# Performance work log

Hardware: AMD Instinct MI355X
Metric: run time of the kernel (lower is better)

The kernel has to match this reference:

```python
import jax, jax.numpy as jnp
import numpy as np

GRID_SIZE = 5
SPLINE_ORDER = 3
NUM_BASIS = GRID_SIZE + SPLINE_ORDER  # 8
GRID = jnp.linspace(-1.0, 1.0, GRID_SIZE + 2 * SPLINE_ORDER + 1)  # [12]
EPS = 1e-6


def bspline_basis(x):
    """Iterative Cox-de Boor. x: [...]; returns [..., NUM_BASIS]."""
    xe = x[..., None]
    # order-0 indicator basis: [..., G-1]
    B = ((xe >= GRID[:-1]) & (xe < GRID[1:])).astype(x.dtype)
    for k in range(1, SPLINE_ORDER + 1):
        nb = B.shape[-1] - 1
        g_i = GRID[:nb]
        g_i1 = GRID[1:1 + nb]
        g_ik = GRID[k:k + nb]
        g_ik1 = GRID[k + 1:k + 1 + nb]
        dl = g_ik - g_i
        dr = g_ik1 - g_i1
        left = jnp.where(dl > EPS, (xe - g_i) / jnp.where(dl > EPS, dl, 1.0), 0.0) * B[..., :nb]
        right = jnp.where(dr > EPS, (g_ik1 - xe) / jnp.where(dr > EPS, dr, 1.0), 0.0) * B[..., 1:nb + 1]
        B = left + right
    return B[..., :NUM_BASIS]


def setup_inputs() -> dict:
    key = jax.random.key(0)
    k1, k2 = jax.random.split(key)
    x = jax.random.normal(k1, (8192, 512), dtype=jnp.float32)
    spline_coeffs = jax.random.normal(k2, (512, 512, NUM_BASIS), dtype=jnp.float32) * 0.1
    return {"x": x, "spline_coeffs": spline_coeffs}


def reference(x, spline_coeffs):
    xn = jnp.tanh(x)                       # [B, in]
    basis = bspline_basis(xn)              # [B, in, K]
    # output[b, o] = sum_{i,k} coeffs[o, i, k] * basis[b, i, k]
    return jnp.einsum('bik,oik->bo', basis, spline_coeffs)
```

## Files before the change

kernel.cpp:

```cpp
#include <hip/hip_runtime.h>
#include <hip/hip_bf16.h>
#include <stdint.h>


#define M_TOTAL 8192
#define N_DIM   512
#define K_DIM   4096
#define BM 128
#define BN 128
#define BK 64
#define NT_HALF 32
#define GRP_LDS 65536
#define BUF_HALF 32768

typedef __attribute__((ext_vector_type(8))) short short8;
typedef __attribute__((ext_vector_type(4))) float f32x4;

typedef const __attribute__((address_space(1))) uint32_t ga_u32;
typedef __attribute__((address_space(3))) uint32_t ls_u32;

__device__ __forceinline__ void gload_lds16(const void* g, void* l) {
  __builtin_amdgcn_global_load_lds((ga_u32*)(uintptr_t)g,
                                   (ls_u32*)(uint32_t)(uintptr_t)l, 16, 0, 0);
}

__device__ __forceinline__ uint32_t f2bf(float f) {
  uint32_t u = __builtin_bit_cast(uint32_t, f);
  return (u + 0x7FFFu + ((u >> 16) & 1u)) >> 16;
}

__device__ __forceinline__ void basis_slots(float xv, uint32_t o[4]) {
  xv = fminf(15.f, fmaxf(-15.f, xv));
  float e  = __expf(2.0f * xv);
  float t  = (e - 1.0f) * __builtin_amdgcn_rcpf(e + 1.0f);
  float uf = (t + 1.0f) * 5.5f;
  int   c  = (int)uf;  c = c > 10 ? 10 : c;
  float u  = uf - (float)c;
  float u2 = u * u, u3 = u2 * u, om = 1.0f - u;
  float w0 = om * om * om * (1.0f / 6.0f);
  float w1 = (3.0f * u3 - 6.0f * u2 + 4.0f) * (1.0f / 6.0f);
  float w2 = (-3.0f * u3 + 3.0f * u2 + 3.0f * u + 1.0f) * (1.0f / 6.0f);
  float w3 = u3 * (1.0f / 6.0f);
  uint32_t p01 = f2bf(w0) | (f2bf(w1) << 16);
  uint32_t p23 = f2bf(w2) | (f2bf(w3) << 16);
  uint64_t W = (uint64_t)p01 | ((uint64_t)p23 << 32);
  int d = c - 3;
  uint64_t lo = (d < 0) ? (W >> ((-d) * 16))
              : ((d < 4) ? (W << (d * 16)) : 0ull);
  uint64_t hi = (d <= 0) ? 0ull
              : ((d < 4) ? (W >> ((4 - d) * 16)) : (W << ((d - 4) * 16)));
  o[0] = (uint32_t)lo; o[1] = (uint32_t)(lo >> 32);
  o[2] = (uint32_t)hi; o[3] = (uint32_t)(hi >> 32);
}

__global__ __launch_bounds__(256) void basis_kernel(const float* __restrict__ x,
                                                    __hip_bfloat16* __restrict__ A,
                                                    int total) {
  int idx = blockIdx.x * 256 + threadIdx.x;
  if (idx >= total) return;
  uint32_t o[4];
  basis_slots(x[idx], o);
  reinterpret_cast<int4*>(A)[idx] = make_int4(o[0], o[1], o[2], o[3]);
}

__global__ __launch_bounds__(256) void cvt_kernel(const float* __restrict__ c,
                                                  __hip_bfloat16* __restrict__ Bt,
                                                  int total8) {
  int idx = blockIdx.x * 256 + threadIdx.x;
  if (idx >= total8) return;
  const float4* cp = reinterpret_cast<const float4*>(c) + (size_t)idx * 2;
  float4 a = cp[0], b = cp[1];
  union { unsigned short us[8]; int4 v; } pk;
  pk.us[0] = (unsigned short)f2bf(a.x); pk.us[1] = (unsigned short)f2bf(a.y);
  pk.us[2] = (unsigned short)f2bf(a.z); pk.us[3] = (unsigned short)f2bf(a.w);
  pk.us[4] = (unsigned short)f2bf(b.x); pk.us[5] = (unsigned short)f2bf(b.y);
  pk.us[6] = (unsigned short)f2bf(b.z); pk.us[7] = (unsigned short)f2bf(b.w);
  reinterpret_cast<int4*>(Bt)[idx] = pk.v;
}

__global__ __launch_bounds__(512) void gemm_kernel(
    const __hip_bfloat16* __restrict__ A,
    const __hip_bfloat16* __restrict__ Bt,
    float* __restrict__ C) {
  __shared__ char lds[2 * GRP_LDS];

  const int tid   = threadIdx.x;
  const int wid   = tid >> 6;
  const int lane  = tid & 63;
  const int quad  = lane >> 4;
  const int l16   = lane & 15;
  const int kgrp  = wid >> 2;
  const int w2    = wid & 3;
  const int waveM = w2 >> 1, waveN = w2 & 1;
  const int tg    = tid & 255;

  const int b  = blockIdx.x;
  const int q  = b >> 3;
  const int mt = (b & 7) * 8 + (q >> 2);
  const int nt = q & 3;
  const int m0 = mt * BM;
  const int n0 = nt * BN;

  char* grp = lds + kgrp * GRP_LDS;

  uint32_t aGlob[4], bGlob[4], sOff[4];
#pragma unroll
  for (int t = 0; t < 4; ++t) {
    int s = t * 256 + tg, row = s >> 3, p = s & 7, cc = p ^ (row & 7);
    sOff[t]  = (uint32_t)s * 16u;
    aGlob[t] = (uint32_t)(m0 + row) * K_DIM + (uint32_t)cc * 8u
             + (uint32_t)kgrp * 2048u;
    bGlob[t] = (uint32_t)(n0 + row) * K_DIM + (uint32_t)cc * 8u
             + (uint32_t)kgrp * 2048u;
  }

  uint32_t aOff[2][4], bOff[2][4];
#pragma unroll
  for (int kk = 0; kk < 2; ++kk) {
    int c = kk * 4 + quad;
#pragma unroll
    for (int mi = 0; mi < 4; ++mi) {
      int row = waveM * 64 + mi * 16 + l16;
      aOff[kk][mi] = (uint32_t)(row * 8 + (c ^ (row & 7))) * 16u;
    }
#pragma unroll
    for (int ni = 0; ni < 4; ++ni) {
      int row = waveN * 64 + ni * 16 + l16;
      bOff[kk][ni] = 16384u + (uint32_t)(row * 8 + (c ^ (row & 7))) * 16u;
    }
  }

  f32x4 acc[4][4];
#pragma unroll
  for (int mi = 0; mi < 4; ++mi)
#pragma unroll
    for (int ni = 0; ni < 4; ++ni)
      acc[mi][ni] = (f32x4){0.f, 0.f, 0.f, 0.f};

#pragma unroll
  for (int t = 0; t < 4; ++t) {
    gload_lds16(A + aGlob[t], grp + sOff[t]);
    gload_lds16(Bt + bGlob[t], grp + 16384 + sOff[t]);
  }

  for (int it = 0; it < NT_HALF; ++it) {
    const int cur = it & 1;
    char* bufc = grp + cur * BUF_HALF;
    __syncthreads();
    if (it + 1 < NT_HALF) {
      char* bufn = grp + (1 - cur) * BUF_HALF;
      uint32_t kt = (uint32_t)(it + 1) * BK;
#pragma unroll
      for (int t = 0; t < 4; ++t) {
        gload_lds16(A + aGlob[t] + kt, bufn + sOff[t]);
        gload_lds16(Bt + bGlob[t] + kt, bufn + 16384 + sOff[t]);
      }
    }
#pragma unroll
    for (int kk = 0; kk < 2; ++kk) {
      short8 af[4], bf[4];
#pragma unroll
      for (int mi = 0; mi < 4; ++mi)
        af[mi] = *reinterpret_cast<const short8*>(bufc + aOff[kk][mi]);
#pragma unroll
      for (int ni = 0; ni < 4; ++ni)
        bf[ni] = *reinterpret_cast<const short8*>(bufc + bOff[kk][ni]);
#pragma unroll
      for (int mi = 0; mi < 4; ++mi)
#pragma unroll
        for (int ni = 0; ni < 4; ++ni)
          acc[mi][ni] = __builtin_amdgcn_mfma_f32_16x16x32_bf16(
              af[mi], bf[ni], acc[mi][ni], 0, 0, 0);
    }
  }

  __syncthreads();
  if (kgrp == 1) {
#pragma unroll
    for (int mi = 0; mi < 4; ++mi)
#pragma unroll
      for (int ni = 0; ni < 4; ++ni) {
        int f = mi * 4 + ni;
        *reinterpret_cast<f32x4*>(lds + w2 * 16384 + f * 1024 + lane * 16) =
            acc[mi][ni];
      }
  }
  __syncthreads();
  if (kgrp == 0) {
#pragma unroll
    for (int mi = 0; mi < 4; ++mi) {
#pragma unroll
      for (int ni = 0; ni < 4; ++ni) {
        int f = mi * 4 + ni;
        f32x4 other = *reinterpret_cast<f32x4*>(
            lds + w2 * 16384 + f * 1024 + lane * 16);
        f32x4 s = acc[mi][ni] + other;
        int col = n0 + waveN * 64 + ni * 16 + l16;
#pragma unroll
        for (int r = 0; r < 4; ++r) {
          int row = m0 + waveM * 64 + mi * 16 + quad * 4 + r;
          C[(size_t)row * N_DIM + col] = s[r];
        }
      }
    }
  }
}

extern "C" void kernel_launch(void* const* d_in, const int* in_sizes, int n_in,
                              void* d_out, int out_size, void* d_ws, size_t ws_size,
                              hipStream_t stream) {
  const float* x    = (const float*)d_in[0];
  const float* coef = (const float*)d_in[1];
  float* out = (float*)d_out;

  __hip_bfloat16* Bt = (__hip_bfloat16*)d_ws;
  __hip_bfloat16* A  = (__hip_bfloat16*)((char*)d_ws + (size_t)4 * 1024 * 1024);

  const int total8 = N_DIM * K_DIM / 8;
  cvt_kernel<<<(total8 + 255) / 256, 256, 0, stream>>>(coef, Bt, total8);

  const int total = M_TOTAL * 512;
  basis_kernel<<<total / 256, 256, 0, stream>>>(x, A, total);

  gemm_kernel<<<(M_TOTAL / BM) * (N_DIM / BN), 512, 0, stream>>>(A, Bt, out);
}
```

Baseline: 118.2 us.

## Use 256x256 tiles with 4-way split-K, interleaved prefetch, and a separate reduce

The GEMM moves from 128x128 tiles with an in-block two-group K split to 256x256 tiles with a 4-way split-K across blocks. Each block writes fp32 partial sums to workspace, and a new reduce kernel adds them. The main loop splits each K step into four MFMA phases, with global-to-LDS prefetch spread between phases and s_setprio around the MFMAs to overlap loads with compute. This aims for higher arithmetic intensity and better latency hiding. The cost is 64 MB of partial-sum traffic plus an extra kernel launch, and higher register pressure from 128 accumulators per thread.

```diff
diff --git a/kernel.cpp b/kernel.cpp
--- a/kernel.cpp
+++ b/kernel.cpp
@@ -6,12 +6,12 @@
 #define M_TOTAL 8192
 #define N_DIM   512
 #define K_DIM   4096
-#define BM 128
-#define BN 128
+#define BM 256
+#define BN 256
 #define BK 64
-#define NT_HALF 32
-#define GRP_LDS 65536
-#define BUF_HALF 32768
+#define NSPLIT 4
+#define NT 16
+#define BUF_SZ 65536
 
 typedef __attribute__((ext_vector_type(8))) short short8;
 typedef __attribute__((ext_vector_type(4))) float f32x4;
@@ -78,131 +78,191 @@
   reinterpret_cast<int4*>(Bt)[idx] = pk.v;
 }
 
-__global__ __launch_bounds__(512) void gemm_kernel(
+__global__ __launch_bounds__(512, 2) void gemm_kernel(
     const __hip_bfloat16* __restrict__ A,
     const __hip_bfloat16* __restrict__ Bt,
-    float* __restrict__ C) {
-  __shared__ char lds[2 * GRP_LDS];
+    float* __restrict__ P) {
+  __shared__ char lds[2 * BUF_SZ];
 
   const int tid   = threadIdx.x;
   const int wid   = tid >> 6;
   const int lane  = tid & 63;
   const int quad  = lane >> 4;
   const int l16   = lane & 15;
-  const int kgrp  = wid >> 2;
-  const int w2    = wid & 3;
-  const int waveM = w2 >> 1, waveN = w2 & 1;
-  const int tg    = tid & 255;
-
-  const int b  = blockIdx.x;
-  const int q  = b >> 3;
-  const int mt = (b & 7) * 8 + (q >> 2);
-  const int nt = q & 3;
+  const int waveM = wid >> 2;
+  const int waveN = wid & 3;
+
+  const int b     = blockIdx.x;
+  const int xcd   = b & 7;
+  const int r     = b >> 3;
+  const int mt    = xcd * 4 + (r >> 3);
+  const int q     = r & 7;
+  const int nt    = q & 1;
+  const int split = q >> 1;
   const int m0 = mt * BM;
   const int n0 = nt * BN;
-
-  char* grp = lds + kgrp * GRP_LDS;
-
-  uint32_t aGlob[4], bGlob[4], sOff[4];
+  const uint32_t kb = (uint32_t)split * 1024u;
+
+  uint32_t aSrc[4], aDst[4], bSrc[4], bDst[4];
 #pragma unroll
   for (int t = 0; t < 4; ++t) {
-    int s = t * 256 + tg, row = s >> 3, p = s & 7, cc = p ^ (row & 7);
-    sOff[t]  = (uint32_t)s * 16u;
-    aGlob[t] = (uint32_t)(m0 + row) * K_DIM + (uint32_t)cc * 8u
-             + (uint32_t)kgrp * 2048u;
-    bGlob[t] = (uint32_t)(n0 + row) * K_DIM + (uint32_t)cc * 8u
-             + (uint32_t)kgrp * 2048u;
-  }
-
-  uint32_t aOff[2][4], bOff[2][4];
+    int p    = tid & 7;
+    int arow = ((t & 1) << 7) + ((t >> 1) << 6) + (tid >> 3);
+    aSrc[t] = (uint32_t)(m0 + arow) * K_DIM + (uint32_t)((p ^ (arow & 7)) * 8)
+            + kb;
+    aDst[t] = (uint32_t)(arow * 8 + p) * 16u;
+    int brow = t * 64 + (tid >> 3);
+    bSrc[t] = (uint32_t)(n0 + brow) * K_DIM + (uint32_t)((p ^ (brow & 7)) * 8)
+            + kb;
+    bDst[t] = 32768u + (uint32_t)(brow * 8 + p) * 16u;
+  }
+
+  uint32_t aOff[2][2][4], bOff[2][4];
 #pragma unroll
   for (int kk = 0; kk < 2; ++kk) {
     int c = kk * 4 + quad;
 #pragma unroll
-    for (int mi = 0; mi < 4; ++mi) {
-      int row = waveM * 64 + mi * 16 + l16;
-      aOff[kk][mi] = (uint32_t)(row * 8 + (c ^ (row & 7))) * 16u;
-    }
+    for (int mh = 0; mh < 2; ++mh)
+#pragma unroll
+      for (int mi = 0; mi < 4; ++mi) {
+        int row = waveM * 128 + mh * 64 + mi * 16 + l16;
+        aOff[kk][mh][mi] = (uint32_t)(row * 8 + (c ^ (row & 7))) * 16u;
+      }
 #pragma unroll
     for (int ni = 0; ni < 4; ++ni) {
       int row = waveN * 64 + ni * 16 + l16;
-      bOff[kk][ni] = 16384u + (uint32_t)(row * 8 + (c ^ (row & 7))) * 16u;
-    }
-  }
-
-  f32x4 acc[4][4];
-#pragma unroll
-  for (int mi = 0; mi < 4; ++mi)
+      bOff[kk][ni] = 32768u + (uint32_t)(row * 8 + (c ^ (row & 7))) * 16u;
+    }
+  }
+
+  f32x4 acc[2][4][4];
+#pragma unroll
+  for (int mh = 0; mh < 2; ++mh)
+#pragma unroll
+    for (int mi = 0; mi < 4; ++mi)
+#pragma unroll
+      for (int ni = 0; ni < 4; ++ni)
+        acc[mh][mi][ni] = (f32x4){0.f, 0.f, 0.f, 0.f};
+
+#pragma unroll
+  for (int t = 0; t < 4; ++t) gload_lds16(Bt + bSrc[t], lds + bDst[t]);
+#pragma unroll
+  for (int t = 0; t < 4; ++t) gload_lds16(A + aSrc[t], lds + aDst[t]);
+  asm volatile("s_waitcnt vmcnt(2)" ::: "memory");
+  __builtin_amdgcn_s_barrier();
+
+  for (int it = 0; it < NT; ++it) {
+    char* bufc = lds + (it & 1) * BUF_SZ;
+    char* bufn = lds + ((it + 1) & 1) * BUF_SZ;
+    const uint32_t kt = (uint32_t)(it + 1) * BK;
+    const bool more = (it + 1) < NT;
+    short8 af[4], bfr[4];
+
+#pragma unroll
+    for (int mi = 0; mi < 4; ++mi)
+      af[mi] = *reinterpret_cast<const short8*>(bufc + aOff[0][0][mi]);
 #pragma unroll
     for (int ni = 0; ni < 4; ++ni)
-      acc[mi][ni] = (f32x4){0.f, 0.f, 0.f, 0.f};
-
-#pragma unroll
-  for (int t = 0; t < 4; ++t) {
-    gload_lds16(A + aGlob[t], grp + sOff[t]);
-    gload_lds16(Bt + bGlob[t], grp + 16384 + sOff[t]);
-  }
-
-  for (int it = 0; it < NT_HALF; ++it) {
-    const int cur = it & 1;
-    char* bufc = grp + cur * BUF_HALF;
-    __syncthreads();
-    if (it + 1 < NT_HALF) {
-      char* bufn = grp + (1 - cur) * BUF_HALF;
-      uint32_t kt = (uint32_t)(it + 1) * BK;
-#pragma unroll
-      for (int t = 0; t < 4; ++t) {
-        gload_lds16(A + aGlob[t] + kt, bufn + sOff[t]);
-        gload_lds16(Bt + bGlob[t] + kt, bufn + 16384 + sOff[t]);
+      bfr[ni] = *reinterpret_cast<const short8*>(bufc + bOff[0][ni]);
+    if (more) {
+      gload_lds16(Bt + bSrc[0] + kt, bufn + bDst[0]);
+      gload_lds16(Bt + bSrc[1] + kt, bufn + bDst[1]);
+      asm volatile("s_waitcnt vmcnt(2)" ::: "memory");
+    } else {
+      asm volatile("s_waitcnt vmcnt(0)" ::: "memory");
+    }
+    __builtin_amdgcn_s_barrier();
+    __builtin_amdgcn_s_setprio(1);
+#pragma unroll
+    for (int mi = 0; mi < 4; ++mi)
+#pragma unroll
+      for (int ni = 0; ni < 4; ++ni)
+        acc[0][mi][ni] = __builtin_amdgcn_mfma_f32_16x16x32_bf16(
+            af[mi], bfr[ni], acc[0][mi][ni], 0, 0, 0);
+    __builtin_amdgcn_s_setprio(0);
+    __builtin_amdgcn_s_barrier();
+
+#pragma unroll
+    for (int mi = 0; mi < 4; ++mi)
+      af[mi] = *reinterpret_cast<const short8*>(bufc + aOff[0][1][mi]);
+    if (more) {
+      gload_lds16(Bt + bSrc[2] + kt, bufn + bDst[2]);
+      gload_lds16(Bt + bSrc[3] + kt, bufn + bDst[3]);
+    }
+    __builtin_amdgcn_s_barrier();
+    __builtin_amdgcn_s_setprio(1);
+#pragma unroll
+    for (int mi = 0; mi < 4; ++mi)
+#pragma unroll
+      for (int ni = 0; ni < 4; ++ni)
+        acc[1][mi][ni] = __builtin_amdgcn_mfma_f32_16x16x32_bf16(
+            af[mi], bfr[ni], acc[1][mi][ni], 0, 0, 0);
+    __builtin_amdgcn_s_setprio(0);
+    __builtin_amdgcn_s_barrier();
+
+#pragma unroll
+    for (int mi = 0; mi < 4; ++mi)
+      af[mi] = *reinterpret_cast<const short8*>(bufc + aOff[1][0][mi]);
+#pragma unroll
+    for (int ni = 0; ni < 4; ++ni)
+      bfr[ni] = *reinterpret_cast<const short8*>(bufc + bOff[1][ni]);
+    if (more) {
+      gload_lds16(A + aSrc[0] + kt, bufn + aDst[0]);
+      gload_lds16(A + aSrc[1] + kt, bufn + aDst[1]);
+    }
+    __builtin_amdgcn_s_barrier();
+    __builtin_amdgcn_s_setprio(1);
+#pragma unroll
+    for (int mi = 0; mi < 4; ++mi)
+#pragma unroll
+      for (int ni = 0; ni < 4; ++ni)
+        acc[0][mi][ni] = __builtin_amdgcn_mfma_f32_16x16x32_bf16(
+            af[mi], bfr[ni], acc[0][mi][ni], 0, 0, 0);
+    __builtin_amdgcn_s_setprio(0);
+    __builtin_amdgcn_s_barrier();
+
+#pragma unroll
+    for (int mi = 0; mi < 4; ++mi)
+      af[mi] = *reinterpret_cast<const short8*>(bufc + aOff[1][1][mi]);
+    if (more) {
+      gload_lds16(A + aSrc[2] + kt, bufn + aDst[2]);
+      gload_lds16(A + aSrc[3] + kt, bufn + aDst[3]);
+      asm volatile("s_waitcnt vmcnt(2)" ::: "memory");
+    }
+    __builtin_amdgcn_s_barrier();
+    __builtin_amdgcn_s_setprio(1);
+#pragma unroll
+    for (int mi = 0; mi < 4; ++mi)
+#pragma unroll
+      for (int ni = 0; ni < 4; ++ni)
+        acc[1][mi][ni] = __builtin_amdgcn_mfma_f32_16x16x32_bf16(
+            af[mi], bfr[ni], acc[1][mi][ni], 0, 0, 0);
+    __builtin_amdgcn_s_setprio(0);
+    __builtin_amdgcn_s_barrier();
+  }
+
+  float* Pb = P + (size_t)split * M_TOTAL * N_DIM;
+#pragma unroll
+  for (int mh = 0; mh < 2; ++mh)
+#pragma unroll
+    for (int mi = 0; mi < 4; ++mi) {
+#pragma unroll
+      for (int ni = 0; ni < 4; ++ni) {
+        int col  = n0 + waveN * 64 + ni * 16 + l16;
+        int rowb = m0 + waveM * 128 + mh * 64 + mi * 16 + quad * 4;
+#pragma unroll
+        for (int rr = 0; rr < 4; ++rr)
+          Pb[(size_t)(rowb + rr) * N_DIM + col] = acc[mh][mi][ni][rr];
       }
     }
-#pragma unroll
-    for (int kk = 0; kk < 2; ++kk) {
-      short8 af[4], bf[4];
-#pragma unroll
-      for (int mi = 0; mi < 4; ++mi)
-        af[mi] = *reinterpret_cast<const short8*>(bufc + aOff[kk][mi]);
-#pragma unroll
-      for (int ni = 0; ni < 4; ++ni)
-        bf[ni] = *reinterpret_cast<const short8*>(bufc + bOff[kk][ni]);
-#pragma unroll
-      for (int mi = 0; mi < 4; ++mi)
-#pragma unroll
-        for (int ni = 0; ni < 4; ++ni)
-          acc[mi][ni] = __builtin_amdgcn_mfma_f32_16x16x32_bf16(
-              af[mi], bf[ni], acc[mi][ni], 0, 0, 0);
-    }
-  }
-
-  __syncthreads();
-  if (kgrp == 1) {
-#pragma unroll
-    for (int mi = 0; mi < 4; ++mi)
-#pragma unroll
-      for (int ni = 0; ni < 4; ++ni) {
-        int f = mi * 4 + ni;
-        *reinterpret_cast<f32x4*>(lds + w2 * 16384 + f * 1024 + lane * 16) =
-            acc[mi][ni];
-      }
-  }
-  __syncthreads();
-  if (kgrp == 0) {
-#pragma unroll
-    for (int mi = 0; mi < 4; ++mi) {
-#pragma unroll
-      for (int ni = 0; ni < 4; ++ni) {
-        int f = mi * 4 + ni;
-        f32x4 other = *reinterpret_cast<f32x4*>(
-            lds + w2 * 16384 + f * 1024 + lane * 16);
-        f32x4 s = acc[mi][ni] + other;
-        int col = n0 + waveN * 64 + ni * 16 + l16;
-#pragma unroll
-        for (int r = 0; r < 4; ++r) {
-          int row = m0 + waveM * 64 + mi * 16 + quad * 4 + r;
-          C[(size_t)row * N_DIM + col] = s[r];
-        }
-      }
-    }
+}
+
+__global__ __launch_bounds__(256) void reduce_kernel(
+    const f32x4* __restrict__ P, f32x4* __restrict__ C, int n4) {
+  const int stride = gridDim.x * 256;
+  for (int i = blockIdx.x * 256 + threadIdx.x; i < n4; i += stride) {
+    f32x4 v = P[i] + P[n4 + i] + P[2 * n4 + i] + P[3 * n4 + i];
+    C[i] = v;
   }
 }
 
@@ -214,7 +274,8 @@
   float* out = (float*)d_out;
 
   __hip_bfloat16* Bt = (__hip_bfloat16*)d_ws;
-  __hip_bfloat16* A  = (__hip_bfloat16*)((char*)d_ws + (size_t)4 * 1024 * 1024);
+  __hip_bfloat16* A  = (__hip_bfloat16*)((char*)d_ws + ((size_t)4 << 20));
+  float*          Pp = (float*)((char*)d_ws + ((size_t)68 << 20));
 
   const int total8 = N_DIM * K_DIM / 8;
   cvt_kernel<<<(total8 + 255) / 256, 256, 0, stream>>>(coef, Bt, total8);
@@ -222,5 +283,8 @@
   const int total = M_TOTAL * 512;
   basis_kernel<<<total / 256, 256, 0, stream>>>(x, A, total);
 
-  gemm_kernel<<<(M_TOTAL / BM) * (N_DIM / BN), 512, 0, stream>>>(A, Bt, out);
-}
+  gemm_kernel<<<256, 512, 0, stream>>>(A, Bt, Pp);
+
+  const int n4 = M_TOTAL * N_DIM / 4;
+  reduce_kernel<<<2048, 256, 0, stream>>>((const f32x4*)Pp, (f32x4*)out, n4);
+}
```

After: 129.9 us. 9.9% more time.
